# Kernel optimization log

Measured on AMD Instinct MI355X. Metric: run time of the kernel, lower is better.

## Reference

```python
import jax, jax.numpy as jnp
import numpy as np

N_NODES = 50000
N_EDGES = 800000
DIMS = [128, 512, 256, 128]
EPS = 1e-5


def setup_inputs() -> dict:
    key = jax.random.key(0)
    ks = jax.random.split(key, 2 + 5 * 3)
    inp = {
        "x": jax.random.normal(ks[0], (N_NODES, DIMS[0]), dtype=jnp.float32),
        "edge_index": jax.random.randint(ks[1], (2, N_EDGES), 0, N_NODES, dtype=jnp.int64),
    }
    ki = 2
    for i in range(3):
        din, dout = DIMS[i], DIMS[i + 1]
        s = 1.0 / np.sqrt(din)
        inp[f"Wl{i}"] = jax.random.uniform(ks[ki + 0], (din, dout), jnp.float32, -s, s)
        inp[f"bl{i}"] = jax.random.uniform(ks[ki + 1], (dout,), jnp.float32, -s, s)
        inp[f"Wr{i}"] = jax.random.uniform(ks[ki + 2], (din, dout), jnp.float32, -s, s)
        inp[f"g{i}"] = jnp.ones((dout,), jnp.float32)
        inp[f"b{i}"] = jnp.zeros((dout,), jnp.float32)
        ki += 5
    return inp


def _sage_mean(x, src, dst, Wl, bl, Wr):
    n = x.shape[0]
    agg = jax.ops.segment_sum(x[src], dst, num_segments=n)  # [N, din]
    deg = jax.ops.segment_sum(jnp.ones((src.shape[0],), x.dtype), dst, num_segments=n)
    mean = agg / jnp.maximum(deg, 1.0)[:, None]
    return mean @ Wl + bl + x @ Wr


def _bn(h, gamma, beta):
    m = h.mean(axis=0)
    v = h.var(axis=0)
    return gamma * (h - m) * jax.lax.rsqrt(v + EPS) + beta


def reference(x, edge_index, Wl0, bl0, Wr0, g0, b0, Wl1, bl1, Wr1, g1, b1, Wl2, bl2, Wr2, g2, b2):
    src, dst = edge_index[0], edge_index[1]
    params = [(Wl0, bl0, Wr0, g0, b0), (Wl1, bl1, Wr1, g1, b1), (Wl2, bl2, Wr2, g2, b2)]
    h = x
    for Wl, bl, Wr, g, b in params:
        h = _sage_mean(h, src, dst, Wl, bl, Wr)
        h = _bn(h, g, b)
        h = jax.nn.relu(h)
        # dropout: identity in eval mode
    return h
```

## Files before the change

kernel.cpp:

```cpp
#include <hip/hip_runtime.h>
#include <cstdint>
#include <cstddef>


#define EPS_BN 1e-5f

typedef unsigned short ushort_t;
typedef __attribute__((ext_vector_type(8))) short short8;
typedef __attribute__((ext_vector_type(4))) float float4v;

__device__ __forceinline__ float bflo(unsigned int w) {
    union { unsigned int i; float f; } v; v.i = w << 16; return v.f;
}
__device__ __forceinline__ float bfhi(unsigned int w) {
    union { unsigned int i; float f; } v; v.i = w & 0xffff0000u; return v.f;
}
__device__ __forceinline__ ushort_t f2bf(float f) {
    union { float f; unsigned int i; } v; v.f = f;
    unsigned int r = v.i + 0x7fffu + ((v.i >> 16) & 1u);
    return (ushort_t)(r >> 16);
}

__device__ __forceinline__ void async_copy16(void* lds, const void* g) {
    __builtin_amdgcn_global_load_lds(
        (const __attribute__((address_space(1))) unsigned int*)g,
        (__attribute__((address_space(3))) unsigned int*)lds, 16, 0, 0);
}

__device__ __forceinline__ void edge_sd(const int* __restrict__ p, int e, int ne,
                                        bool is64, int& s, int& d) {
    if (is64) { s = p[2 * e];  d = p[2 * ne + 2 * e]; }
    else      { s = p[e];      d = p[ne + e]; }
}
__device__ __forceinline__ int edge_d(const int* __restrict__ p, int e, int ne, bool is64) {
    return is64 ? p[2 * ne + 2 * e] : p[ne + e];
}

__device__ __forceinline__ bool detect_is64(const int* __restrict__ edges,
                                            int* sh_flag, int t) {
    if (t == 0) *sh_flag = 1;
    __syncthreads();
    if (t < 64 && edges[2 * t + 1] != 0) *sh_flag = 0;
    __syncthreads();
    return *sh_flag != 0;
}

#define EPB 2048

__global__ __launch_bounds__(256) void bhist_kernel(
    const int* __restrict__ edges, int ne, int* __restrict__ gcnt) {
    __shared__ int h[256];
    __shared__ int f64;
    int t = threadIdx.x;
    bool is64 = detect_is64(edges, &f64, t);
    h[t] = 0;
    __syncthreads();
    int base_e = blockIdx.x * EPB;
    #pragma unroll
    for (int u = 0; u < EPB / 256; ++u) {
        int i = base_e + u * 256 + t;
        if (i < ne) atomicAdd(&h[edge_d(edges, i, ne, is64) >> 8], 1);
    }
    __syncthreads();
    if (h[t]) atomicAdd(&gcnt[t], h[t]);
}

__global__ __launch_bounds__(256) void bscan_kernel(
    const int* __restrict__ gcnt, int nb, int ne,
    int* __restrict__ bbase, int* __restrict__ bcur) {
    __shared__ int sh[256];
    int t = threadIdx.x;
    int v = (t < nb) ? gcnt[t] : 0;
    sh[t] = v;
    __syncthreads();
    for (int o = 1; o < 256; o <<= 1) {
        int x = (t >= o) ? sh[t - o] : 0;
        __syncthreads();
        sh[t] += x;
        __syncthreads();
    }
    int excl = sh[t] - v;
    if (t < nb) { bbase[t] = excl; bcur[t] = excl; }
    if (t == nb) bbase[t] = ne;
    if (t == 0 && nb == 256) bbase[256] = ne;
}

__global__ __launch_bounds__(256) void bscatter_kernel(
    const int* __restrict__ edges, int ne,
    int* __restrict__ bcur, int* __restrict__ packed) {
    __shared__ int h[256];
    __shared__ int chunkb[256];
    __shared__ int lcur[256];
    __shared__ int f64;
    int t = threadIdx.x;
    bool is64 = detect_is64(edges, &f64, t);
    h[t] = 0;
    lcur[t] = 0;
    __syncthreads();
    int base_e = blockIdx.x * EPB;
    int ent[EPB / 256], eb[EPB / 256];
    #pragma unroll
    for (int u = 0; u < EPB / 256; ++u) {
        int i = base_e + u * 256 + t;
        if (i < ne) {
            int s, d;
            edge_sd(edges, i, ne, is64, s, d);
            ent[u] = s | ((d & 255) << 24);
            eb[u] = d >> 8;
            atomicAdd(&h[eb[u]], 1);
        } else eb[u] = -1;
    }
    __syncthreads();
    if (h[t]) chunkb[t] = atomicAdd(&bcur[t], h[t]);
    __syncthreads();
    #pragma unroll
    for (int u = 0; u < EPB / 256; ++u) {
        if (eb[u] >= 0) {
            int lp = atomicAdd(&lcur[eb[u]], 1);
            packed[chunkb[eb[u]] + lp] = ent[u];
        }
    }
}

__global__ __launch_bounds__(256) void bbuild_kernel(
    const int* __restrict__ packed, const int* __restrict__ bbase,
    int* __restrict__ rowptr, int* __restrict__ csr_src, int n) {
    __shared__ int h[256];
    __shared__ int cur[256];
    int t = threadIdx.x;
    int bb = blockIdx.x;
    int base = bbase[bb], cnt = bbase[bb + 1] - base;
    h[t] = 0;
    __syncthreads();
    for (int i = t; i < cnt; i += 256)
        atomicAdd(&h[(unsigned)packed[base + i] >> 24], 1);
    __syncthreads();
    int v = h[t];
    for (int o = 1; o < 256; o <<= 1) {
        int x = (t >= o) ? h[t - o] : 0;
        __syncthreads();
        h[t] += x;
        __syncthreads();
    }
    int excl = h[t] - v;
    int node = bb * 256 + t;
    if (node <= n) rowptr[node] = base + excl;
    cur[t] = excl;
    __syncthreads();
    for (int i = t; i < cnt; i += 256) {
        int e = packed[base + i];
        int lp = atomicAdd(&cur[(unsigned)e >> 24], 1);
        csr_src[base + lp] = e & 0xffffff;
    }
}

__global__ void prep_all_kernel(
    const float* __restrict__ x, ushort_t* __restrict__ xb, int nxb,
    const float* __restrict__ Wl0, const float* __restrict__ Wr0,
    ushort_t* __restrict__ WT0, int nb0,
    const float* __restrict__ Wl1, const float* __restrict__ Wr1,
    ushort_t* __restrict__ WT1c, int nb1,
    const float* __restrict__ Wl2, const float* __restrict__ Wr2,
    ushort_t* __restrict__ WT2c) {
    const int D0 = 128, D1 = 512, D2 = 256, D3 = 128;
    int b = blockIdx.x;
    if (b < nxb) {
        int i = b * 256 + threadIdx.x;
        xb[i] = f2bf(x[i]);
        return;
    }
    b -= nxb;
    if (b < nb0) {
        int idx = b * 256 + threadIdx.x;
        int K2 = 2 * D0;
        int nn = idx / K2, k = idx - nn * K2;
        float v = (k < D0) ? Wl0[(size_t)k * D1 + nn] : Wr0[(size_t)(k - D0) * D1 + nn];
        WT0[idx] = f2bf(v);
        return;
    }
    b -= nb0;
    if (b < nb1) {
        int idx = b * 256 + threadIdx.x;
        int nn = idx / D1, k = idx - nn * D1;
        float v = (nn < D2) ? Wl1[(size_t)k * D2 + nn] : Wr1[(size_t)k * D2 + (nn - D2)];
        WT1c[idx] = f2bf(v);
        return;
    }
    b -= nb1;
    {
        int idx = b * 256 + threadIdx.x;
        int nn = idx / D2, k = idx - nn * D2;
        float v = (nn < D3) ? Wl2[(size_t)k * D3 + nn] : Wr2[(size_t)k * D3 + (nn - D3)];
        WT2c[idx] = f2bf(v);
    }
}

template <int VEC> struct VecT;
template <> struct VecT<2> { using T = unsigned int; };
template <> struct VecT<4> { using T = uint2; };
template <> struct VecT<8> { using T = uint4; };

template <int VEC>
__device__ __forceinline__ void vunpack(typename VecT<VEC>::T v, unsigned int* w) {
    if constexpr (VEC == 2) { w[0] = v; }
    else if constexpr (VEC == 4) { w[0] = v.x; w[1] = v.y; }
    else { w[0] = v.x; w[1] = v.y; w[2] = v.z; w[3] = v.w; }
}

template <int VEC>
__device__ __forceinline__ void vaccum(typename VecT<VEC>::T v, float* acc) {
    unsigned int w[VEC / 2];
    vunpack<VEC>(v, w);
    #pragma unroll
    for (int i = 0; i < VEC / 2; ++i) {
        acc[2 * i + 0] += bflo(w[i]);
        acc[2 * i + 1] += bfhi(w[i]);
    }
}

template <int VEC>
__device__ __forceinline__ void gather_sum(
    const ushort_t* __restrict__ base, const int* __restrict__ csr_src,
    int e0, int e1, int rstride, float* acc) {
    using VT = typename VecT<VEC>::T;
    int e = e0;
    for (; e + 16 <= e1; e += 16) {
        VT v[16];
        #pragma unroll
        for (int u = 0; u < 16; ++u)
            v[u] = *(const VT*)(base + (size_t)csr_src[e + u] * rstride);
        #pragma unroll
        for (int u = 0; u < 16; ++u) vaccum<VEC>(v[u], acc);
    }
    if (e + 8 <= e1) {
        VT v[8];
        #pragma unroll
        for (int u = 0; u < 8; ++u)
            v[u] = *(const VT*)(base + (size_t)csr_src[e + u] * rstride);
        #pragma unroll
        for (int u = 0; u < 8; ++u) vaccum<VEC>(v[u], acc);
        e += 8;
    }
    if (e + 4 <= e1) {
        VT v[4];
        #pragma unroll
        for (int u = 0; u < 4; ++u)
            v[u] = *(const VT*)(base + (size_t)csr_src[e + u] * rstride);
        #pragma unroll
        for (int u = 0; u < 4; ++u) vaccum<VEC>(v[u], acc);
        e += 4;
    }
    if (e + 2 <= e1) {
        VT v0 = *(const VT*)(base + (size_t)csr_src[e] * rstride);
        VT v1 = *(const VT*)(base + (size_t)csr_src[e + 1] * rstride);
        vaccum<VEC>(v0, acc); vaccum<VEC>(v1, acc);
        e += 2;
    }
    if (e < e1)
        vaccum<VEC>(*(const VT*)(base + (size_t)csr_src[e] * rstride), acc);
}

template <int VEC>
__global__ __launch_bounds__(256) void aggregate_wave_kernel(
    const ushort_t* __restrict__ h, ushort_t* __restrict__ mean,
    const int* __restrict__ rowptr, const int* __restrict__ csr_src, int nnodes) {
    const int din = VEC * 64;
    int wid = blockIdx.x * 4 + (threadIdx.x >> 6);
    if (wid >= nnodes) return;
    int lane = threadIdx.x & 63;
    int e0 = rowptr[wid], e1 = rowptr[wid + 1];

    float acc[VEC];
    #pragma unroll
    for (int i = 0; i < VEC; ++i) acc[i] = 0.f;
    gather_sum<VEC>(h + (size_t)lane * VEC, csr_src, e0, e1, din, acc);

    int deg = e1 - e0;
    float scale = 1.0f / (float)(deg > 1 ? deg : 1);
    unsigned int o[VEC / 2];
    #pragma unroll
    for (int i = 0; i < VEC / 2; ++i)
        o[i] = (unsigned int)f2bf(acc[2 * i] * scale) |
               ((unsigned int)f2bf(acc[2 * i + 1] * scale) << 16);
    using VT = typename VecT<VEC>::T;
    VT ov;
    if constexpr (VEC == 2) { ov = o[0]; }
    else if constexpr (VEC == 4) { ov.x = o[0]; ov.y = o[1]; }
    else { ov.x = o[0]; ov.y = o[1]; ov.z = o[2]; ov.w = o[3]; }
    *(VT*)(mean + (size_t)wid * din + (size_t)lane * VEC) = ov;
}

template <int VEC>
__global__ __launch_bounds__(256) void aggregate_add_kernel(
    const ushort_t* __restrict__ PR, const float* __restrict__ bias,
    ushort_t* __restrict__ pre,
    const int* __restrict__ rowptr, const int* __restrict__ csr_src, int nnodes) {
    const int D = VEC * 64;
    const int stride = 2 * D;
    int wid = blockIdx.x * 4 + (threadIdx.x >> 6);
    if (wid >= nnodes) return;
    int lane = threadIdx.x & 63;
    int e0 = rowptr[wid], e1 = rowptr[wid + 1];

    float acc[VEC];
    #pragma unroll
    for (int i = 0; i < VEC; ++i) acc[i] = 0.f;
    gather_sum<VEC>(PR + (size_t)lane * VEC, csr_src, e0, e1, stride, acc);

    int deg = e1 - e0;
    float scale = 1.0f / (float)(deg > 1 ? deg : 1);

    using VT = typename VecT<VEC>::T;
    VT rv = *(const VT*)(PR + (size_t)wid * stride + D + (size_t)lane * VEC);
    unsigned int rw[VEC / 2];
    vunpack<VEC>(rv, rw);
    float o[VEC];
    #pragma unroll
    for (int i = 0; i < VEC / 2; ++i) {
        o[2 * i + 0] = bflo(rw[i]);
        o[2 * i + 1] = bfhi(rw[i]);
    }
    #pragma unroll
    for (int i = 0; i < VEC; ++i)
        o[i] += acc[i] * scale + bias[lane * VEC + i];

    unsigned int ow[VEC / 2];
    #pragma unroll
    for (int i = 0; i < VEC / 2; ++i)
        ow[i] = (unsigned int)f2bf(o[2 * i]) | ((unsigned int)f2bf(o[2 * i + 1]) << 16);
    VT ov;
    if constexpr (VEC == 2) { ov = ow[0]; }
    else if constexpr (VEC == 4) { ov.x = ow[0]; ov.y = ow[1]; }
    else { ov.x = ow[0]; ov.y = ow[1]; ov.z = ow[2]; ov.w = ow[3]; }
    *(VT*)(pre + (size_t)wid * D + (size_t)lane * VEC) = ov;
}

template <bool DUAL, bool BIAS>
__global__ __launch_bounds__(512) void gemm_glds_kernel(
    const ushort_t* __restrict__ A1, const ushort_t* __restrict__ A2,
    const ushort_t* __restrict__ BT, const float* __restrict__ bias,
    ushort_t* __restrict__ Cb, int N, int K1, int Ktot, int Wtot) {
    __shared__ ushort_t As[256 * 64];
    __shared__ ushort_t Bs[128 * 64];

    const int tid = threadIdx.x;
    const int wave = tid >> 6;
    const int lane = tid & 63;
    const int quad = lane >> 4;
    const int l15 = lane & 15;
    const int sw7 = l15 & 7;
    const int rowBase = blockIdx.y * 256;
    const int colBase = blockIdx.x * 128;
    const int wm = (wave >> 1) * 64;
    const int wn = (wave & 1) * 64;

    float4v acc[4][4];
    #pragma unroll
    for (int i = 0; i < 4; ++i)
        #pragma unroll
        for (int j = 0; j < 4; ++j)
            acc[i][j] = (float4v){0.f, 0.f, 0.f, 0.f};

    const int nkt = Ktot / 64;
    const int khalf = K1 / 64;

    for (int kt = 0; kt < nkt; ++kt) {
        const ushort_t* Asrc = A1;
        int kg = kt * 64;
        if (DUAL && kt >= khalf) { Asrc = A2; kg = (kt - khalf) * 64; }
        const int kb = kt * 64;

        #pragma unroll
        for (int u = 0; u < 4; ++u) {
            int c = u * 512 + tid;
            int r = c >> 3, cc = c & 7;
            int off = (cc ^ (r & 7)) * 8;
            int grow = rowBase + r;
            if (grow >= N) grow = N - 1;
            async_copy16(&As[c * 8], Asrc + (size_t)grow * K1 + kg + off);
        }
        #pragma unroll
        for (int u = 0; u < 2; ++u) {
            int c = u * 512 + tid;
            int r = c >> 3, cc = c & 7;
            int off = (cc ^ (r & 7)) * 8;
            async_copy16(&Bs[c * 8], BT + (size_t)(colBase + r) * Ktot + kb + off);
        }
        __syncthreads();

        #pragma unroll
        for (int kh = 0; kh < 2; ++kh) {
            int cidx = kh * 4 + quad;
            short8 af[4], bf4[4];
            #pragma unroll
            for (int i = 0; i < 4; ++i)
                af[i] = *(const short8*)&As[(wm + i * 16 + l15) * 64 + (cidx ^ sw7) * 8];
            #pragma unroll
            for (int j = 0; j < 4; ++j)
                bf4[j] = *(const short8*)&Bs[(wn + j * 16 + l15) * 64 + (cidx ^ sw7) * 8];
            #pragma unroll
            for (int i = 0; i < 4; ++i)
                #pragma unroll
                for (int j = 0; j < 4; ++j)
                    acc[i][j] = __builtin_amdgcn_mfma_f32_16x16x32_bf16(bf4[j], af[i], acc[i][j], 0, 0, 0);
        }
        __syncthreads();
    }

    ushort_t* lws = &As[wave * 2048];
    #pragma unroll
    for (int p = 0; p < 2; ++p) {
        #pragma unroll
        for (int jj = 0; jj < 2; ++jj) {
            int j = 2 * p + jj;
            float4 bv = make_float4(0.f, 0.f, 0.f, 0.f);
            if (BIAS) bv = *(const float4*)(bias + colBase + wn + j * 16 + quad * 4);
            #pragma unroll
            for (int i = 0; i < 4; ++i) {
                uint2 pk;
                pk.x = (unsigned int)f2bf(acc[i][j][0] + bv.x) |
                       ((unsigned int)f2bf(acc[i][j][1] + bv.y) << 16);
                pk.y = (unsigned int)f2bf(acc[i][j][2] + bv.z) |
                       ((unsigned int)f2bf(acc[i][j][3] + bv.w) << 16);
                *(uint2*)&lws[(i * 16 + l15) * 32 + jj * 16 + quad * 4] = pk;
            }
        }
        __syncthreads();
        #pragma unroll
        for (int it = 0; it < 4; ++it) {
            int c = it * 64 + lane;
            int row = c >> 2, coff = (c & 3) * 8;
            int grow = rowBase + wm + row;
            if (grow < N) {
                uint4 v = *(const uint4*)&lws[row * 32 + coff];
                *(uint4*)(Cb + (size_t)grow * Wtot + colBase + wn + p * 32 + coff) = v;
            }
        }
        __syncthreads();
    }
}

__global__ void colstats_b_kernel(const ushort_t* __restrict__ h, int N, int D,
                                  float* __restrict__ sum, float* __restrict__ sumsq) {
    int c2 = blockIdx.x * 128 + (threadIdx.x & 63) * 2;
    int rl = threadIdx.x >> 6;
    float s0 = 0.f, s20 = 0.f, s1 = 0.f, s21 = 0.f;
    int stride = gridDim.y * 4;
    for (int r = blockIdx.y * 4 + rl; r < N; r += stride) {
        unsigned int w = *(const unsigned int*)(h + (size_t)r * D + c2);
        float v0 = bflo(w), v1 = bfhi(w);
        s0 += v0; s20 += v0 * v0;
        s1 += v1; s21 += v1 * v1;
    }
    atomicAdd(&sum[c2 + 0], s0);
    atomicAdd(&sumsq[c2 + 0], s20);
    atomicAdd(&sum[c2 + 1], s1);
    atomicAdd(&sumsq[c2 + 1], s21);
}

__global__ void bn_relu_b2b_kernel(const ushort_t* __restrict__ h, ushort_t* __restrict__ hb,
                                   int N, int D,
                                   const float* __restrict__ sum, const float* __restrict__ sumsq,
                                   const float* __restrict__ g, const float* __restrict__ b) {
    size_t idx = (size_t)blockIdx.x * blockDim.x + threadIdx.x;
    size_t tot = (size_t)N * D / 2;
    if (idx >= tot) return;
    int cp = (int)(idx & (size_t)(D / 2 - 1));
    int c0 = cp * 2, c1 = c0 + 1;
    float m0 = sum[c0] / (float)N, m1 = sum[c1] / (float)N;
    float i0 = rsqrtf(sumsq[c0] / (float)N - m0 * m0 + EPS_BN);
    float i1 = rsqrtf(sumsq[c1] / (float)N - m1 * m1 + EPS_BN);
    unsigned int w = ((const unsigned int*)h)[idx];
    float v0 = g[c0] * (bflo(w) - m0) * i0 + b[c0];
    float v1 = g[c1] * (bfhi(w) - m1) * i1 + b[c1];
    v0 = v0 > 0.f ? v0 : 0.f;
    v1 = v1 > 0.f ? v1 : 0.f;
    ((unsigned int*)hb)[idx] = (unsigned int)f2bf(v0) | ((unsigned int)f2bf(v1) << 16);
}

__global__ void bn_relu_b2f_kernel(const ushort_t* __restrict__ h, float* __restrict__ hf,
                                   int N, int D,
                                   const float* __restrict__ sum, const float* __restrict__ sumsq,
                                   const float* __restrict__ g, const float* __restrict__ b) {
    size_t idx = (size_t)blockIdx.x * blockDim.x + threadIdx.x;
    size_t tot = (size_t)N * D / 2;
    if (idx >= tot) return;
    int cp = (int)(idx & (size_t)(D / 2 - 1));
    int c0 = cp * 2, c1 = c0 + 1;
    float m0 = sum[c0] / (float)N, m1 = sum[c1] / (float)N;
    float i0 = rsqrtf(sumsq[c0] / (float)N - m0 * m0 + EPS_BN);
    float i1 = rsqrtf(sumsq[c1] / (float)N - m1 * m1 + EPS_BN);
    unsigned int w = ((const unsigned int*)h)[idx];
    float v0 = g[c0] * (bflo(w) - m0) * i0 + b[c0];
    float v1 = g[c1] * (bfhi(w) - m1) * i1 + b[c1];
    float2 o;
    o.x = v0 > 0.f ? v0 : 0.f;
    o.y = v1 > 0.f ? v1 : 0.f;
    *(float2*)(hf + idx * 2) = o;
}

extern "C" void kernel_launch(void* const* d_in, const int* in_sizes, int n_in,
                              void* d_out, int out_size, void* d_ws, size_t ws_size,
                              hipStream_t stream) {
    const float* x     = (const float*)d_in[0];
    const int*   edges = (const int*)d_in[1];
    const float* Wl0 = (const float*)d_in[2];
    const float* bl0 = (const float*)d_in[3];
    const float* Wr0 = (const float*)d_in[4];
    const float* g0  = (const float*)d_in[5];
    const float* b0  = (const float*)d_in[6];
    const float* Wl1 = (const float*)d_in[7];
    const float* bl1 = (const float*)d_in[8];
    const float* Wr1 = (const float*)d_in[9];
    const float* g1  = (const float*)d_in[10];
    const float* b1  = (const float*)d_in[11];
    const float* Wl2 = (const float*)d_in[12];
    const float* bl2 = (const float*)d_in[13];
    const float* Wr2 = (const float*)d_in[14];
    const float* g2  = (const float*)d_in[15];
    const float* b2  = (const float*)d_in[16];

    const int D0 = 128, D1 = 512, D2 = 256, D3 = 128;
    const int n  = in_sizes[0] / D0;
    const int ne = in_sizes[1] / 2;
    const int NB = (n + 255) >> 8;

    char* base = (char*)d_ws;
    size_t off = 0;
    auto alloc = [&](size_t bytes) -> char* {
        char* p = base + off;
        off = (off + bytes + 255) & ~(size_t)255;
        return p;
    };
    int*      gcnt    = (int*)alloc(256 * 4);
    float*    stats   = (float*)alloc(6 * 512 * 4);
    size_t    zero_span = off;
    int*      bbase   = (int*)alloc(257 * 4);
    int*      bcur    = (int*)alloc(256 * 4);
    int*      packed  = (int*)alloc((size_t)ne * 4);
    int*      rowptr  = (int*)alloc((size_t)(n + 1) * 4);
    int*      csr_src = (int*)alloc((size_t)ne * 4);
    ushort_t* xb      = (ushort_t*)alloc((size_t)n * D0 * 2);
    ushort_t* mb      = (ushort_t*)alloc((size_t)n * 512 * 2);
    ushort_t* h1b     = (ushort_t*)alloc((size_t)n * D1 * 2);
    ushort_t* h2b     = (ushort_t*)alloc((size_t)n * D2 * 2);
    ushort_t* hpre    = (ushort_t*)alloc((size_t)n * 512 * 2);
    ushort_t* WT0     = (ushort_t*)alloc((size_t)D1 * 2 * D0 * 2);
    ushort_t* WT1c    = (ushort_t*)alloc((size_t)(2 * D2) * D1 * 2);
    ushort_t* WT2c    = (ushort_t*)alloc((size_t)(2 * D3) * D2 * 2);
    float*    out     = (float*)d_out;
    (void)ws_size; (void)n_in; (void)out_size;

    hipMemsetAsync(base, 0, zero_span, stream);

    int ablk = (ne + EPB - 1) / EPB;
    bhist_kernel<<<ablk, 256, 0, stream>>>(edges, ne, gcnt);
    bscan_kernel<<<1, 256, 0, stream>>>(gcnt, NB, ne, bbase, bcur);
    bscatter_kernel<<<ablk, 256, 0, stream>>>(edges, ne, bcur, packed);
    bbuild_kernel<<<NB, 256, 0, stream>>>(packed, bbase, rowptr, csr_src, n);

    const int nxb = (n * D0) / 256;
    const int nb0 = (D1 * 2 * D0) / 256;
    const int nb1 = (2 * D2 * D1) / 256;
    const int nb2 = (2 * D3 * D2) / 256;
    prep_all_kernel<<<nxb + nb0 + nb1 + nb2, 256, 0, stream>>>(
        x, xb, nxb, Wl0, Wr0, WT0, nb0, Wl1, Wr1, WT1c, nb1, Wl2, Wr2, WT2c);

    const int aggGrid = (n + 3) / 4;
    const int rowBlocks = (n + 255) / 256;
    float* st0 = stats + 0 * 1024;
    float* st1 = stats + 1 * 1024;
    float* st2 = stats + 2 * 1024;

    aggregate_wave_kernel<2><<<aggGrid, 256, 0, stream>>>(xb, mb, rowptr, csr_src, n);
    gemm_glds_kernel<true, true><<<dim3(D1 / 128, rowBlocks), 512, 0, stream>>>(
        mb, xb, WT0, bl0, hpre, n, D0, 2 * D0, D1);
    colstats_b_kernel<<<dim3(D1 / 128, 128), 256, 0, stream>>>(hpre, n, D1, st0, st0 + 512);
    bn_relu_b2b_kernel<<<((size_t)n * D1 / 2 + 255) / 256, 256, 0, stream>>>(
        hpre, h1b, n, D1, st0, st0 + 512, g0, b0);

    gemm_glds_kernel<false, false><<<dim3(2 * D2 / 128, rowBlocks), 512, 0, stream>>>(
        h1b, nullptr, WT1c, nullptr, mb, n, D1, D1, 2 * D2);
    aggregate_add_kernel<4><<<aggGrid, 256, 0, stream>>>(
        mb, bl1, hpre, rowptr, csr_src, n);
    colstats_b_kernel<<<dim3(D2 / 128, 128), 256, 0, stream>>>(hpre, n, D2, st1, st1 + 512);
    bn_relu_b2b_kernel<<<((size_t)n * D2 / 2 + 255) / 256, 256, 0, stream>>>(
        hpre, h2b, n, D2, st1, st1 + 512, g1, b1);

    gemm_glds_kernel<false, false><<<dim3(2 * D3 / 128, rowBlocks), 512, 0, stream>>>(
        h2b, nullptr, WT2c, nullptr, mb, n, D2, D2, 2 * D3);
    aggregate_add_kernel<2><<<aggGrid, 256, 0, stream>>>(
        mb, bl2, hpre, rowptr, csr_src, n);
    colstats_b_kernel<<<dim3(D3 / 128, 128), 256, 0, stream>>>(hpre, n, D3, st2, st2 + 512);
    bn_relu_b2f_kernel<<<((size_t)n * D3 / 2 + 255) / 256, 256, 0, stream>>>(
        hpre, out, n, D3, st2, st2 + 512, g2, b2);
}
```

Measured before the change: 578.5 us.

## Fuse BatchNorm column statistics into GEMM and aggregation epilogues

Removes the separate colstats kernels by accumulating per-column sum and sum-of-squares inside the GEMM epilogue (layer 0) and inside a grid-stride aggregate_add kernel (layers 1-2), then atomically adding them to global buffers. Aggregation kernels become persistent grid-stride loops with a fixed grid of 2048 blocks. Nontemporal loads and stores are added for streaming reads and writes. Statistics are now taken from fp32 values before bf16 rounding, and the extra register and atomic pressure could affect GEMM occupancy.

```diff
diff --git a/kernel.cpp b/kernel.cpp
--- a/kernel.cpp
+++ b/kernel.cpp
@@ -8,6 +8,9 @@
 typedef unsigned short ushort_t;
 typedef __attribute__((ext_vector_type(8))) short short8;
 typedef __attribute__((ext_vector_type(4))) float float4v;
+typedef __attribute__((ext_vector_type(2))) float float2v;
+typedef __attribute__((ext_vector_type(2))) unsigned int uint2v;
+typedef __attribute__((ext_vector_type(4))) unsigned int uint4v;
 
 __device__ __forceinline__ float bflo(unsigned int w) {
     union { unsigned int i; float f; } v; v.i = w << 16; return v.f;
@@ -197,8 +200,8 @@
 
 template <int VEC> struct VecT;
 template <> struct VecT<2> { using T = unsigned int; };
-template <> struct VecT<4> { using T = uint2; };
-template <> struct VecT<8> { using T = uint4; };
+template <> struct VecT<4> { using T = uint2v; };
+template <> struct VecT<8> { using T = uint4v; };
 
 template <int VEC>
 __device__ __forceinline__ void vunpack(typename VecT<VEC>::T v, unsigned int* w) {
@@ -265,81 +268,108 @@
     const ushort_t* __restrict__ h, ushort_t* __restrict__ mean,
     const int* __restrict__ rowptr, const int* __restrict__ csr_src, int nnodes) {
     const int din = VEC * 64;
-    int wid = blockIdx.x * 4 + (threadIdx.x >> 6);
-    if (wid >= nnodes) return;
-    int lane = threadIdx.x & 63;
-    int e0 = rowptr[wid], e1 = rowptr[wid + 1];
-
-    float acc[VEC];
-    #pragma unroll
-    for (int i = 0; i < VEC; ++i) acc[i] = 0.f;
-    gather_sum<VEC>(h + (size_t)lane * VEC, csr_src, e0, e1, din, acc);
-
-    int deg = e1 - e0;
-    float scale = 1.0f / (float)(deg > 1 ? deg : 1);
-    unsigned int o[VEC / 2];
-    #pragma unroll
-    for (int i = 0; i < VEC / 2; ++i)
-        o[i] = (unsigned int)f2bf(acc[2 * i] * scale) |
-               ((unsigned int)f2bf(acc[2 * i + 1] * scale) << 16);
+    const int wave = threadIdx.x >> 6;
+    const int lane = threadIdx.x & 63;
+    const int wstride = gridDim.x * 4;
     using VT = typename VecT<VEC>::T;
-    VT ov;
-    if constexpr (VEC == 2) { ov = o[0]; }
-    else if constexpr (VEC == 4) { ov.x = o[0]; ov.y = o[1]; }
-    else { ov.x = o[0]; ov.y = o[1]; ov.z = o[2]; ov.w = o[3]; }
-    *(VT*)(mean + (size_t)wid * din + (size_t)lane * VEC) = ov;
+    for (int wid = blockIdx.x * 4 + wave; wid < nnodes; wid += wstride) {
+        int e0 = rowptr[wid], e1 = rowptr[wid + 1];
+        float acc[VEC];
+        #pragma unroll
+        for (int i = 0; i < VEC; ++i) acc[i] = 0.f;
+        gather_sum<VEC>(h + (size_t)lane * VEC, csr_src, e0, e1, din, acc);
+
+        int deg = e1 - e0;
+        float scale = 1.0f / (float)(deg > 1 ? deg : 1);
+        unsigned int o[VEC / 2];
+        #pragma unroll
+        for (int i = 0; i < VEC / 2; ++i)
+            o[i] = (unsigned int)f2bf(acc[2 * i] * scale) |
+                   ((unsigned int)f2bf(acc[2 * i + 1] * scale) << 16);
+        VT ov;
+        if constexpr (VEC == 2) { ov = o[0]; }
+        else if constexpr (VEC == 4) { ov.x = o[0]; ov.y = o[1]; }
+        else { ov.x = o[0]; ov.y = o[1]; ov.z = o[2]; ov.w = o[3]; }
+        *(VT*)(mean + (size_t)wid * din + (size_t)lane * VEC) = ov;
+    }
 }
 
 template <int VEC>
 __global__ __launch_bounds__(256) void aggregate_add_kernel(
     const ushort_t* __restrict__ PR, const float* __restrict__ bias,
     ushort_t* __restrict__ pre,
-    const int* __restrict__ rowptr, const int* __restrict__ csr_src, int nnodes) {
+    const int* __restrict__ rowptr, const int* __restrict__ csr_src, int nnodes,
+    float* __restrict__ gsum, float* __restrict__ gsq) {
     const int D = VEC * 64;
     const int stride = 2 * D;
-    int wid = blockIdx.x * 4 + (threadIdx.x >> 6);
-    if (wid >= nnodes) return;
-    int lane = threadIdx.x & 63;
-    int e0 = rowptr[wid], e1 = rowptr[wid + 1];
-
-    float acc[VEC];
-    #pragma unroll
-    for (int i = 0; i < VEC; ++i) acc[i] = 0.f;
-    gather_sum<VEC>(PR + (size_t)lane * VEC, csr_src, e0, e1, stride, acc);
-
-    int deg = e1 - e0;
-    float scale = 1.0f / (float)(deg > 1 ? deg : 1);
-
+    __shared__ float s_red[2][4][VEC * 64];
+    const int wave = threadIdx.x >> 6;
+    const int lane = threadIdx.x & 63;
+    const int wstride = gridDim.x * 4;
     using VT = typename VecT<VEC>::T;
-    VT rv = *(const VT*)(PR + (size_t)wid * stride + D + (size_t)lane * VEC);
-    unsigned int rw[VEC / 2];
-    vunpack<VEC>(rv, rw);
-    float o[VEC];
-    #pragma unroll
-    for (int i = 0; i < VEC / 2; ++i) {
-        o[2 * i + 0] = bflo(rw[i]);
-        o[2 * i + 1] = bfhi(rw[i]);
-    }
-    #pragma unroll
-    for (int i = 0; i < VEC; ++i)
-        o[i] += acc[i] * scale + bias[lane * VEC + i];
-
-    unsigned int ow[VEC / 2];
-    #pragma unroll
-    for (int i = 0; i < VEC / 2; ++i)
-        ow[i] = (unsigned int)f2bf(o[2 * i]) | ((unsigned int)f2bf(o[2 * i + 1]) << 16);
-    VT ov;
-    if constexpr (VEC == 2) { ov = ow[0]; }
-    else if constexpr (VEC == 4) { ov.x = ow[0]; ov.y = ow[1]; }
-    else { ov.x = ow[0]; ov.y = ow[1]; ov.z = ow[2]; ov.w = ow[3]; }
-    *(VT*)(pre + (size_t)wid * D + (size_t)lane * VEC) = ov;
-}
-
-template <bool DUAL, bool BIAS>
+
+    float ssum[VEC], ssq[VEC];
+    #pragma unroll
+    for (int i = 0; i < VEC; ++i) { ssum[i] = 0.f; ssq[i] = 0.f; }
+
+    for (int wid = blockIdx.x * 4 + wave; wid < nnodes; wid += wstride) {
+        int e0 = rowptr[wid], e1 = rowptr[wid + 1];
+        float acc[VEC];
+        #pragma unroll
+        for (int i = 0; i < VEC; ++i) acc[i] = 0.f;
+        gather_sum<VEC>(PR + (size_t)lane * VEC, csr_src, e0, e1, stride, acc);
+
+        int deg = e1 - e0;
+        float scale = 1.0f / (float)(deg > 1 ? deg : 1);
+
+        VT rv = __builtin_nontemporal_load((const VT*)(PR + (size_t)wid * stride + D + (size_t)lane * VEC));
+        unsigned int rw[VEC / 2];
+        vunpack<VEC>(rv, rw);
+        float o[VEC];
+        #pragma unroll
+        for (int i = 0; i < VEC / 2; ++i) {
+            o[2 * i + 0] = bflo(rw[i]);
+            o[2 * i + 1] = bfhi(rw[i]);
+        }
+        #pragma unroll
+        for (int i = 0; i < VEC; ++i) {
+            o[i] += acc[i] * scale + bias[lane * VEC + i];
+            ssum[i] += o[i];
+            ssq[i] += o[i] * o[i];
+        }
+
+        unsigned int ow[VEC / 2];
+        #pragma unroll
+        for (int i = 0; i < VEC / 2; ++i)
+            ow[i] = (unsigned int)f2bf(o[2 * i]) | ((unsigned int)f2bf(o[2 * i + 1]) << 16);
+        VT ov;
+        if constexpr (VEC == 2) { ov = ow[0]; }
+        else if constexpr (VEC == 4) { ov.x = ow[0]; ov.y = ow[1]; }
+        else { ov.x = ow[0]; ov.y = ow[1]; ov.z = ow[2]; ov.w = ow[3]; }
+        __builtin_nontemporal_store(ov, (VT*)(pre + (size_t)wid * D + (size_t)lane * VEC));
+    }
+
+    #pragma unroll
+    for (int i = 0; i < VEC; ++i) {
+        s_red[0][wave][lane * VEC + i] = ssum[i];
+        s_red[1][wave][lane * VEC + i] = ssq[i];
+    }
+    __syncthreads();
+    int t = threadIdx.x;
+    if (t < D) {
+        float a = s_red[0][0][t] + s_red[0][1][t] + s_red[0][2][t] + s_red[0][3][t];
+        float q = s_red[1][0][t] + s_red[1][1][t] + s_red[1][2][t] + s_red[1][3][t];
+        atomicAdd(&gsum[t], a);
+        atomicAdd(&gsq[t], q);
+    }
+}
+
+template <bool DUAL, bool BIAS, bool STATS>
 __global__ __launch_bounds__(512) void gemm_glds_kernel(
     const ushort_t* __restrict__ A1, const ushort_t* __restrict__ A2,
     const ushort_t* __restrict__ BT, const float* __restrict__ bias,
-    ushort_t* __restrict__ Cb, int N, int K1, int Ktot, int Wtot) {
+    ushort_t* __restrict__ Cb, int N, int K1, int Ktot, int Wtot,
+    float* __restrict__ gsum, float* __restrict__ gsq) {
     __shared__ ushort_t As[256 * 64];
     __shared__ ushort_t Bs[128 * 64];
 
@@ -407,6 +437,14 @@
         __syncthreads();
     }
 
+    float cs[4][4], cq[4][4];
+    if constexpr (STATS) {
+        #pragma unroll
+        for (int j = 0; j < 4; ++j)
+            #pragma unroll
+            for (int r = 0; r < 4; ++r) { cs[j][r] = 0.f; cq[j][r] = 0.f; }
+    }
+
     ushort_t* lws = &As[wave * 2048];
     #pragma unroll
     for (int p = 0; p < 2; ++p) {
@@ -417,11 +455,21 @@
             if (BIAS) bv = *(const float4*)(bias + colBase + wn + j * 16 + quad * 4);
             #pragma unroll
             for (int i = 0; i < 4; ++i) {
+                float v0 = acc[i][j][0] + bv.x;
+                float v1 = acc[i][j][1] + bv.y;
+                float v2 = acc[i][j][2] + bv.z;
+                float v3 = acc[i][j][3] + bv.w;
+                if constexpr (STATS) {
+                    if (rowBase + wm + i * 16 + l15 < N) {
+                        cs[j][0] += v0; cq[j][0] += v0 * v0;
+                        cs[j][1] += v1; cq[j][1] += v1 * v1;
+                        cs[j][2] += v2; cq[j][2] += v2 * v2;
+                        cs[j][3] += v3; cq[j][3] += v3 * v3;
+                    }
+                }
                 uint2 pk;
-                pk.x = (unsigned int)f2bf(acc[i][j][0] + bv.x) |
-                       ((unsigned int)f2bf(acc[i][j][1] + bv.y) << 16);
-                pk.y = (unsigned int)f2bf(acc[i][j][2] + bv.z) |
-                       ((unsigned int)f2bf(acc[i][j][3] + bv.w) << 16);
+                pk.x = (unsigned int)f2bf(v0) | ((unsigned int)f2bf(v1) << 16);
+                pk.y = (unsigned int)f2bf(v2) | ((unsigned int)f2bf(v3) << 16);
                 *(uint2*)&lws[(i * 16 + l15) * 32 + jj * 16 + quad * 4] = pk;
             }
         }
@@ -438,24 +486,29 @@
         }
         __syncthreads();
     }
-}
-
-__global__ void colstats_b_kernel(const ushort_t* __restrict__ h, int N, int D,
-                                  float* __restrict__ sum, float* __restrict__ sumsq) {
-    int c2 = blockIdx.x * 128 + (threadIdx.x & 63) * 2;
-    int rl = threadIdx.x >> 6;
-    float s0 = 0.f, s20 = 0.f, s1 = 0.f, s21 = 0.f;
-    int stride = gridDim.y * 4;
-    for (int r = blockIdx.y * 4 + rl; r < N; r += stride) {
-        unsigned int w = *(const unsigned int*)(h + (size_t)r * D + c2);
-        float v0 = bflo(w), v1 = bfhi(w);
-        s0 += v0; s20 += v0 * v0;
-        s1 += v1; s21 += v1 * v1;
-    }
-    atomicAdd(&sum[c2 + 0], s0);
-    atomicAdd(&sumsq[c2 + 0], s20);
-    atomicAdd(&sum[c2 + 1], s1);
-    atomicAdd(&sumsq[c2 + 1], s21);
+
+    if constexpr (STATS) {
+        #pragma unroll
+        for (int j = 0; j < 4; ++j)
+            #pragma unroll
+            for (int r = 0; r < 4; ++r) {
+                #pragma unroll
+                for (int m = 1; m < 16; m <<= 1) {
+                    cs[j][r] += __shfl_xor(cs[j][r], m);
+                    cq[j][r] += __shfl_xor(cq[j][r], m);
+                }
+            }
+        if (l15 == 0) {
+            #pragma unroll
+            for (int j = 0; j < 4; ++j)
+                #pragma unroll
+                for (int r = 0; r < 4; ++r) {
+                    int col = colBase + wn + j * 16 + quad * 4 + r;
+                    atomicAdd(&gsum[col], cs[j][r]);
+                    atomicAdd(&gsq[col], cq[j][r]);
+                }
+        }
+    }
 }
 
 __global__ void bn_relu_b2b_kernel(const ushort_t* __restrict__ h, ushort_t* __restrict__ hb,
@@ -470,7 +523,7 @@
     float m0 = sum[c0] / (float)N, m1 = sum[c1] / (float)N;
     float i0 = rsqrtf(sumsq[c0] / (float)N - m0 * m0 + EPS_BN);
     float i1 = rsqrtf(sumsq[c1] / (float)N - m1 * m1 + EPS_BN);
-    unsigned int w = ((const unsigned int*)h)[idx];
+    unsigned int w = __builtin_nontemporal_load(&((const unsigned int*)h)[idx]);
     float v0 = g[c0] * (bflo(w) - m0) * i0 + b[c0];
     float v1 = g[c1] * (bfhi(w) - m1) * i1 + b[c1];
     v0 = v0 > 0.f ? v0 : 0.f;
@@ -490,13 +543,13 @@
     float m0 = sum[c0] / (float)N, m1 = sum[c1] / (float)N;
     float i0 = rsqrtf(sumsq[c0] / (float)N - m0 * m0 + EPS_BN);
     float i1 = rsqrtf(sumsq[c1] / (float)N - m1 * m1 + EPS_BN);
-    unsigned int w = ((const unsigned int*)h)[idx];
+    unsigned int w = __builtin_nontemporal_load(&((const unsigned int*)h)[idx]);
     float v0 = g[c0] * (bflo(w) - m0) * i0 + b[c0];
     float v1 = g[c1] * (bfhi(w) - m1) * i1 + b[c1];
-    float2 o;
+    float2v o;
     o.x = v0 > 0.f ? v0 : 0.f;
     o.y = v1 > 0.f ? v1 : 0.f;
-    *(float2*)(hf + idx * 2) = o;
+    __builtin_nontemporal_store(o, (float2v*)(hf + idx * 2));
 }
 
 extern "C" void kernel_launch(void* const* d_in, const int* in_sizes, int n_in,
@@ -566,32 +619,29 @@
     prep_all_kernel<<<nxb + nb0 + nb1 + nb2, 256, 0, stream>>>(
         x, xb, nxb, Wl0, Wr0, WT0, nb0, Wl1, Wr1, WT1c, nb1, Wl2, Wr2, WT2c);
 
-    const int aggGrid = (n + 3) / 4;
+    const int aggGrid = 2048;
     const int rowBlocks = (n + 255) / 256;
     float* st0 = stats + 0 * 1024;
     float* st1 = stats + 1 * 1024;
     float* st2 = stats + 2 * 1024;
 
     aggregate_wave_kernel<2><<<aggGrid, 256, 0, stream>>>(xb, mb, rowptr, csr_src, n);
-    gemm_glds_kernel<true, true><<<dim3(D1 / 128, rowBlocks), 512, 0, stream>>>(
-        mb, xb, WT0, bl0, hpre, n, D0, 2 * D0, D1);
-    colstats_b_kernel<<<dim3(D1 / 128, 128), 256, 0, stream>>>(hpre, n, D1, st0, st0 + 512);
+    gemm_glds_kernel<true, true, true><<<dim3(D1 / 128, rowBlocks), 512, 0, stream>>>(
+        mb, xb, WT0, bl0, hpre, n, D0, 2 * D0, D1, st0, st0 + 512);
     bn_relu_b2b_kernel<<<((size_t)n * D1 / 2 + 255) / 256, 256, 0, stream>>>(
         hpre, h1b, n, D1, st0, st0 + 512, g0, b0);
 
-    gemm_glds_kernel<false, false><<<dim3(2 * D2 / 128, rowBlocks), 512, 0, stream>>>(
-        h1b, nullptr, WT1c, nullptr, mb, n, D1, D1, 2 * D2);
+    gemm_glds_kernel<false, false, false><<<dim3(2 * D2 / 128, rowBlocks), 512, 0, stream>>>(
+        h1b, nullptr, WT1c, nullptr, mb, n, D1, D1, 2 * D2, nullptr, nullptr);
     aggregate_add_kernel<4><<<aggGrid, 256, 0, stream>>>(
-        mb, bl1, hpre, rowptr, csr_src, n);
-    colstats_b_kernel<<<dim3(D2 / 128, 128), 256, 0, stream>>>(hpre, n, D2, st1, st1 + 512);
+        mb, bl1, hpre, rowptr, csr_src, n, st1, st1 + 512);
     bn_relu_b2b_kernel<<<((size_t)n * D2 / 2 + 255) / 256, 256, 0, stream>>>(
         hpre, h2b, n, D2, st1, st1 + 512, g1, b1);
 
-    gemm_glds_kernel<false, false><<<dim3(2 * D3 / 128, rowBlocks), 512, 0, stream>>>(
-        h2b, nullptr, WT2c, nullptr, mb, n, D2, D2, 2 * D3);
+    gemm_glds_kernel<false, false, false><<<dim3(2 * D3 / 128, rowBlocks), 512, 0, stream>>>(
+        h2b, nullptr, WT2c, nullptr, mb, n, D2, D2, 2 * D3, nullptr, nullptr);
     aggregate_add_kernel<2><<<aggGrid, 256, 0, stream>>>(
-        mb, bl2, hpre, rowptr, csr_src, n);
-    colstats_b_kernel<<<dim3(D3 / 128, 128), 256, 0, stream>>>(hpre, n, D3, st2, st2 + 512);
+        mb, bl2, hpre, rowptr, csr_src, n, st2, st2 + 512);
     bn_relu_b2f_kernel<<<((size_t)n * D3 / 2 + 255) / 256, 256, 0, stream>>>(
         hpre, out, n, D3, st2, st2 + 512, g2, b2);
 }
```

Result: no change. 587.1 us (+1.5%).
